# Kernel optimization log

Hardware: AMD Instinct MI355X
Metric: run time of the kernel (lower is better)

## Reference

```python
import jax, jax.numpy as jnp
import numpy as np

NEG_SLOPE = 0.2

def gatv2(x, edge_index, Wl, bl, Wr, br, att, bias):
    # PyG GATv2Conv (share_weights=False, add_self_loops=True, concat=True)
    N = x.shape[0]
    H, D = att.shape
    src0, dst0 = edge_index[0], edge_index[1]
    # remove_self_loops + add_self_loops semantics: mask existing self loops,
    # append one self loop per node (keeps static shapes under jit)
    loop = jnp.arange(N, dtype=src0.dtype)
    src = jnp.concatenate([src0, loop])
    dst = jnp.concatenate([dst0, loop])
    keep = jnp.concatenate([src0 != dst0, jnp.ones(N, dtype=bool)])  # drop original i->i edges
    xl = (x @ Wl + bl).reshape(N, H, D)  # source-side transform
    xr = (x @ Wr + br).reshape(N, H, D)  # target-side transform
    e = xl[src] + xr[dst]                                  # [E,H,D]
    logits = jnp.einsum('ehd,hd->eh', jax.nn.leaky_relu(e, NEG_SLOPE), att)
    logits = jnp.where(keep[:, None], logits, -jnp.inf)
    m = jax.ops.segment_max(logits, dst, num_segments=N)   # [N,H]
    ex = jnp.where(keep[:, None], jnp.exp(logits - m[dst]), 0.0)
    denom = jax.ops.segment_sum(ex, dst, num_segments=N)   # [N,H]
    alpha = ex / (denom[dst] + 1e-16)                      # [E,H]
    out = jax.ops.segment_sum(alpha[..., None] * xl[src], dst, num_segments=N)
    return out.reshape(N, H * D) + bias

def setup_inputs() -> dict:
    key = jax.random.key(0)
    ks = jax.random.split(key, 20)
    N, E, F, Hd = 50000, 400000, 5, 128
    s = 0.05
    inp = {
        'x': jax.random.normal(ks[0], (N, F), dtype=jnp.float32),
        'edge_index': jax.random.randint(ks[1], (2, E), 0, N, dtype=jnp.int64),
        # node_embed MLP
        'W1': jax.random.normal(ks[2], (F, Hd), dtype=jnp.float32) * s,
        'b1': jnp.zeros((Hd,), jnp.float32),
        'W2': jax.random.normal(ks[3], (Hd, Hd), dtype=jnp.float32) * s,
        'b2': jnp.zeros((Hd,), jnp.float32),
        # gnn1: GATv2Conv(128 -> 128, heads=4)
        'Wl1': jax.random.normal(ks[4], (Hd, 4 * Hd), dtype=jnp.float32) * s,
        'bl1': jnp.zeros((4 * Hd,), jnp.float32),
        'Wr1': jax.random.normal(ks[5], (Hd, 4 * Hd), dtype=jnp.float32) * s,
        'br1': jnp.zeros((4 * Hd,), jnp.float32),
        'att1': jax.random.normal(ks[6], (4, Hd), dtype=jnp.float32) * s,
        'bias1': jnp.zeros((4 * Hd,), jnp.float32),
        # gnn2: GATv2Conv(512 -> 128, heads=1)
        'Wl2': jax.random.normal(ks[7], (4 * Hd, Hd), dtype=jnp.float32) * s,
        'bl2': jnp.zeros((Hd,), jnp.float32),
        'Wr2': jax.random.normal(ks[8], (4 * Hd, Hd), dtype=jnp.float32) * s,
        'br2': jnp.zeros((Hd,), jnp.float32),
        'att2': jax.random.normal(ks[9], (1, Hd), dtype=jnp.float32) * s,
        'bias2': jnp.zeros((Hd,), jnp.float32),
    }
    return inp

def reference(x, edge_index, W1, b1, W2, b2, Wl1, bl1, Wr1, br1, att1, bias1,
              Wl2, bl2, Wr2, br2, att2, bias2):
    h = jax.nn.relu(x @ W1 + b1) @ W2 + b2                 # node_embed MLP
    h = jax.nn.relu(gatv2(h, edge_index, Wl1, bl1, Wr1, br1, att1, bias1))
    out = gatv2(h, edge_index, Wl2, bl2, Wr2, br2, att2, bias2)
    return out  # [N, 128]
```

## Files before the change

### kernel.cpp

```cpp
#include <hip/hip_runtime.h>
#include <math.h>

typedef __attribute__((ext_vector_type(8))) short bf16x8;
typedef __attribute__((ext_vector_type(4))) float f32x4;
typedef unsigned short ushort;
typedef unsigned int uint;

static __device__ __forceinline__ ushort f2bf(float f) {
    unsigned u = __float_as_uint(f);
    u = u + 0x7fff + ((u >> 16) & 1);
    return (ushort)(u >> 16);
}
static __device__ __forceinline__ float bf2f(ushort h) {
    return __uint_as_float(((unsigned)h) << 16);
}


__global__ void k_count(const int* __restrict__ src, const int* __restrict__ dst,
                        int E, int* __restrict__ counts) {
    int e = blockIdx.x * blockDim.x + threadIdx.x;
    if (e < E) {
        int s = src[e], d = dst[e];
        if (s != d) atomicAdd(&counts[d], 1);
    }
}

__global__ __launch_bounds__(256) void k_blocksum(const int* __restrict__ counts, int N,
                                                  int* __restrict__ bsum) {
    __shared__ int s[256];
    int t = threadIdx.x, i = blockIdx.x * 256 + t;
    s[t] = (i < N) ? counts[i] : 0;
    __syncthreads();
    for (int off = 128; off > 0; off >>= 1) {
        if (t < off) s[t] += s[t + off];
        __syncthreads();
    }
    if (t == 0) bsum[blockIdx.x] = s[0];
}

__global__ __launch_bounds__(256) void k_scanblocks(const int* __restrict__ bsum, int NB,
                                                    int* __restrict__ boff,
                                                    int* __restrict__ rowptr, int N) {
    __shared__ int s[256];
    int t = threadIdx.x;
    int v = (t < NB) ? bsum[t] : 0;
    s[t] = v;
    __syncthreads();
    for (int off = 1; off < 256; off <<= 1) {
        int u = (t >= off) ? s[t - off] : 0;
        __syncthreads();
        s[t] += u;
        __syncthreads();
    }
    if (t < NB) boff[t] = s[t] - v;
    if (t == NB - 1) rowptr[N] = s[t] + N;
}

__global__ __launch_bounds__(256) void k_scatter(const int* __restrict__ counts, int N,
                                                 const int* __restrict__ boff,
                                                 int* __restrict__ rowptr,
                                                 int* __restrict__ cursor) {
    __shared__ int s[256];
    int t = threadIdx.x, i = blockIdx.x * 256 + t;
    int c = (i < N) ? counts[i] : 0;
    s[t] = c;
    __syncthreads();
    for (int off = 1; off < 256; off <<= 1) {
        int u = (t >= off) ? s[t - off] : 0;
        __syncthreads();
        s[t] += u;
        __syncthreads();
    }
    if (i < N) {
        int excl = boff[blockIdx.x] + s[t] - c + i;
        rowptr[i] = excl;
        cursor[i] = excl;
    }
}

__global__ void k_fill(const int* __restrict__ src, const int* __restrict__ dst,
                       int E, int N, int* __restrict__ cursor, int* __restrict__ colA) {
    int i = blockIdx.x * blockDim.x + threadIdx.x;
    if (i < E) {
        int s = src[i], d = dst[i];
        if (s != d) { int p = atomicAdd(&cursor[d], 1); colA[p] = s; }
    } else if (i < E + N) {
        int n = i - E;
        int p = atomicAdd(&cursor[n], 1); colA[p] = n;
    }
}


__global__ __launch_bounds__(256) void k_repack(
    const float* __restrict__ W2, const float* __restrict__ Wl1,
    const float* __restrict__ Wr1, const float* __restrict__ Wl2,
    const float* __restrict__ Wr2,
    ushort* __restrict__ wfh, ushort* __restrict__ wfl)
{
    int job = blockIdx.y;
    int t = blockIdx.x * 256 + threadIdx.x;
    int ks = t >> 9, n = (t >> 6) & 7, l = t & 63;

    const float* W; int ldw, rowoff, col0;
    if (job == 0)      { W = W2;  ldw = 128; rowoff = 0;              col0 = 0; }
    else if (job < 5)  { W = Wl1; ldw = 512; rowoff = 0;              col0 = (job - 1) * 128; }
    else if (job < 9)  { W = Wr1; ldw = 512; rowoff = 0;              col0 = (job - 5) * 128; }
    else if (job < 13) { W = Wl2; ldw = 128; rowoff = (job - 9) * 128;  col0 = 0; }
    else               { W = Wr2; ldw = 128; rowoff = (job - 13) * 128; col0 = 0; }

    int krow = rowoff + ks * 32 + (l >> 4) * 8;
    int col = col0 + n * 16 + (l & 15);
    size_t dbase = (size_t)job * 16384 + (((size_t)(ks * 8 + n)) * 64 + l) * 8;
#pragma unroll
    for (int j = 0; j < 8; j++) {
        float v = W[(size_t)(krow + j) * ldw + col];
        ushort h = f2bf(v);
        ushort lo = f2bf(v - bf2f(h));
        wfh[dbase + j] = h;
        wfl[dbase + j] = lo;
    }
}


__global__ __launch_bounds__(256) void k_mlp1(
    const float* __restrict__ x, const float* __restrict__ W1, const float* __restrict__ b1,
    ushort* __restrict__ out, int N)
{
    int n = blockIdx.x * 2 + (threadIdx.x >> 7);
    int j = threadIdx.x & 127;
    if (n >= N) return;
    float s = b1[j];
#pragma unroll
    for (int k = 0; k < 5; k++) s = fmaf(x[(size_t)n * 5 + k], W1[k * 128 + j], s);
    s = fmaxf(s, 0.f);
    out[(size_t)n * 128 + j] = f2bf(s);
}


__global__ __launch_bounds__(256) void gemm_h0(
    const ushort* __restrict__ A,
    const ushort* __restrict__ wfh, const ushort* __restrict__ wfl,
    const float* __restrict__ bias,
    ushort* __restrict__ C, int M)
{
    int tid = threadIdx.x;
    int w = tid >> 6, l = tid & 63;
    int m0 = blockIdx.x * 128 + w * 32;
    int lr = l & 15, kg = l >> 4;

    f32x4 acc[2][8];
#pragma unroll
    for (int i = 0; i < 2; i++)
#pragma unroll
        for (int j = 0; j < 8; j++) acc[i][j] = (f32x4){0.f, 0.f, 0.f, 0.f};

    int row0 = m0 + lr, row1 = m0 + 16 + lr;
    bool ok0 = row0 < M, ok1 = row1 < M;
    const bf16x8 zz = {0, 0, 0, 0, 0, 0, 0, 0};

#pragma unroll
    for (int ks = 0; ks < 4; ks++) {
        int koff = ks * 32 + kg * 8;
        bf16x8 a0 = ok0 ? *(const bf16x8*)(A + (size_t)row0 * 128 + koff) : zz;
        bf16x8 a1 = ok1 ? *(const bf16x8*)(A + (size_t)row1 * 128 + koff) : zz;
#pragma unroll
        for (int n = 0; n < 8; n++) {
            size_t bo = (((size_t)(ks * 8 + n)) * 64 + l) * 8;
            bf16x8 bh = *(const bf16x8*)(wfh + bo);
            bf16x8 bl = *(const bf16x8*)(wfl + bo);
            acc[0][n] = __builtin_amdgcn_mfma_f32_16x16x32_bf16(a0, bh, acc[0][n], 0, 0, 0);
            acc[0][n] = __builtin_amdgcn_mfma_f32_16x16x32_bf16(a0, bl, acc[0][n], 0, 0, 0);
            acc[1][n] = __builtin_amdgcn_mfma_f32_16x16x32_bf16(a1, bh, acc[1][n], 0, 0, 0);
            acc[1][n] = __builtin_amdgcn_mfma_f32_16x16x32_bf16(a1, bl, acc[1][n], 0, 0, 0);
        }
    }

#pragma unroll
    for (int mf = 0; mf < 2; mf++) {
#pragma unroll
        for (int r = 0; r < 4; r++) {
            int row = m0 + mf * 16 + kg * 4 + r;
            if (row >= M) continue;
#pragma unroll
            for (int n = 0; n < 8; n++) {
                size_t idx = (size_t)row * 128 + n * 16 + lr;
                C[idx] = f2bf(acc[mf][n][r] + bias[n * 16 + lr]);
            }
        }
    }
}


__global__ __launch_bounds__(256) void gemm_xlr1(
    const ushort* __restrict__ A,
    const ushort* __restrict__ wh, const ushort* __restrict__ wl,
    const float* __restrict__ bl1, const float* __restrict__ br1,
    ushort* __restrict__ out, int M)
{
    int t = blockIdx.y;
    int tid = threadIdx.x;
    int w = tid >> 6, l = tid & 63;
    int m0 = blockIdx.x * 128 + w * 32;
    int lr = l & 15, kg = l >> 4;

    const ushort* bh_base = wh + (size_t)t * 16384;
    const ushort* bl_base = wl + (size_t)t * 16384;

    f32x4 acc[2][8];
#pragma unroll
    for (int i = 0; i < 2; i++)
#pragma unroll
        for (int j = 0; j < 8; j++) acc[i][j] = (f32x4){0.f, 0.f, 0.f, 0.f};

    int row0 = m0 + lr, row1 = m0 + 16 + lr;
    bool ok0 = row0 < M, ok1 = row1 < M;
    const bf16x8 zz = {0, 0, 0, 0, 0, 0, 0, 0};

#pragma unroll
    for (int ks = 0; ks < 4; ks++) {
        int koff = ks * 32 + kg * 8;
        bf16x8 a0 = ok0 ? *(const bf16x8*)(A + (size_t)row0 * 128 + koff) : zz;
        bf16x8 a1 = ok1 ? *(const bf16x8*)(A + (size_t)row1 * 128 + koff) : zz;
#pragma unroll
        for (int n = 0; n < 8; n++) {
            size_t bo = (((size_t)(ks * 8 + n)) * 64 + l) * 8;
            bf16x8 bh = *(const bf16x8*)(bh_base + bo);
            bf16x8 bl = *(const bf16x8*)(bl_base + bo);
            acc[0][n] = __builtin_amdgcn_mfma_f32_16x16x32_bf16(a0, bh, acc[0][n], 0, 0, 0);
            acc[0][n] = __builtin_amdgcn_mfma_f32_16x16x32_bf16(a0, bl, acc[0][n], 0, 0, 0);
            acc[1][n] = __builtin_amdgcn_mfma_f32_16x16x32_bf16(a1, bh, acc[1][n], 0, 0, 0);
            acc[1][n] = __builtin_amdgcn_mfma_f32_16x16x32_bf16(a1, bl, acc[1][n], 0, 0, 0);
        }
    }

    float bcol[8];
#pragma unroll
    for (int n = 0; n < 8; n++)
        bcol[n] = (t < 4) ? bl1[t * 128 + n * 16 + lr] : br1[(t - 4) * 128 + n * 16 + lr];

#pragma unroll
    for (int mf = 0; mf < 2; mf++) {
#pragma unroll
        for (int r = 0; r < 4; r++) {
            int row = m0 + mf * 16 + kg * 4 + r;
            if (row >= M) continue;
#pragma unroll
            for (int n = 0; n < 8; n++)
                out[(size_t)row * 1024 + t * 128 + n * 16 + lr] = f2bf(acc[mf][n][r] + bcol[n]);
        }
    }
}


__global__ __launch_bounds__(256) void gemm_xlr2(
    const ushort* __restrict__ A,
    const ushort* __restrict__ wfh, const ushort* __restrict__ wfl,
    const float* __restrict__ bl2, const float* __restrict__ br2,
    ushort* __restrict__ xl2, ushort* __restrict__ xr2, int M)
{
    int t = blockIdx.y;
    int tid = threadIdx.x;
    int w = tid >> 6, l = tid & 63;
    int m0 = blockIdx.x * 128 + w * 32;
    int lr = l & 15, kg = l >> 4;

    f32x4 acc[2][8];
#pragma unroll
    for (int i = 0; i < 2; i++)
#pragma unroll
        for (int j = 0; j < 8; j++) acc[i][j] = (f32x4){0.f, 0.f, 0.f, 0.f};

    int row0 = m0 + lr, row1 = m0 + 16 + lr;
    bool ok0 = row0 < M, ok1 = row1 < M;
    const bf16x8 zz = {0, 0, 0, 0, 0, 0, 0, 0};

    for (int kc = 0; kc < 4; kc++) {
        const ushort* bh_base = wfh + (size_t)(9 + t * 4 + kc) * 16384;
        const ushort* bl_base = wfl + (size_t)(9 + t * 4 + kc) * 16384;
        bf16x8 a0[4], a1[4];
#pragma unroll
        for (int ks = 0; ks < 4; ks++) {
            int koff = kc * 128 + ks * 32 + kg * 8;
            a0[ks] = ok0 ? *(const bf16x8*)(A + (size_t)row0 * 512 + koff) : zz;
            a1[ks] = ok1 ? *(const bf16x8*)(A + (size_t)row1 * 512 + koff) : zz;
        }
#pragma unroll
        for (int ks = 0; ks < 4; ks++) {
#pragma unroll
            for (int n = 0; n < 8; n++) {
                size_t bo = (((size_t)(ks * 8 + n)) * 64 + l) * 8;
                bf16x8 bh = *(const bf16x8*)(bh_base + bo);
                bf16x8 bl = *(const bf16x8*)(bl_base + bo);
                acc[0][n] = __builtin_amdgcn_mfma_f32_16x16x32_bf16(a0[ks], bh, acc[0][n], 0, 0, 0);
                acc[0][n] = __builtin_amdgcn_mfma_f32_16x16x32_bf16(a0[ks], bl, acc[0][n], 0, 0, 0);
                acc[1][n] = __builtin_amdgcn_mfma_f32_16x16x32_bf16(a1[ks], bh, acc[1][n], 0, 0, 0);
                acc[1][n] = __builtin_amdgcn_mfma_f32_16x16x32_bf16(a1[ks], bl, acc[1][n], 0, 0, 0);
            }
        }
    }

    const float* bias = (t == 0) ? bl2 : br2;
    ushort* outp = (t == 0) ? xl2 : xr2;

#pragma unroll
    for (int mf = 0; mf < 2; mf++) {
#pragma unroll
        for (int r = 0; r < 4; r++) {
            int row = m0 + mf * 16 + kg * 4 + r;
            if (row >= M) continue;
#pragma unroll
            for (int n = 0; n < 8; n++) {
                int col = n * 16 + lr;
                outp[(size_t)row * 128 + col] = f2bf(acc[mf][n][r] + bias[col]);
            }
        }
    }
}


__global__ __launch_bounds__(256) void gat_edge4(
    const ushort* __restrict__ xlr,
    const float* __restrict__ att,
    const float* __restrict__ bias,
    const int* __restrict__ rowptr, const int* __restrict__ colA,
    ushort* __restrict__ h1,
    int N)
{
    int n = blockIdx.x;
    int h = threadIdx.x >> 6, l = threadIdx.x & 63;
    int g = l >> 4, q = l & 15;

    const ushort* xlbase = xlr + h * 128 + q * 8;

    bf16x8 xrv = *(const bf16x8*)(xlr + (size_t)n * 1024 + (4 + h) * 128 + q * 8);
    float4 ata = *(const float4*)(att + h * 128 + q * 8);
    float4 atb = *(const float4*)(att + h * 128 + q * 8 + 4);
    float xr[8] , at[8] = {ata.x, ata.y, ata.z, ata.w, atb.x, atb.y, atb.z, atb.w};
#pragma unroll
    for (int j = 0; j < 8; j++) xr[j] = bf2f((ushort)xrv[j]);

    auto dotc = [&](bf16x8 v8, float* vv) -> float {
        float c = 0.f;
#pragma unroll
        for (int j = 0; j < 8; j++) {
            vv[j] = bf2f((ushort)v8[j]);
            float t = vv[j] + xr[j];
            t = (t > 0.f) ? t : 0.2f * t;
            c = fmaf(t, at[j], c);
        }
        c += __shfl_xor(c, 1);
        c += __shfl_xor(c, 2);
        c += __shfl_xor(c, 4);
        c += __shfl_xor(c, 8);
        return c;
    };

    float tmp[8];
    bf16x8 vself = *(const bf16x8*)(xlbase + (size_t)n * 1024);
    float cs = dotc(vself, tmp);

    int k0 = rowptr[n], k1 = rowptr[n + 1];
    float s = 0.f, o[8];
#pragma unroll
    for (int j = 0; j < 8; j++) o[j] = 0.f;

    auto edge = [&](bf16x8 v8) {
        float vv[8];
        float c = dotc(v8, vv);
        float p = __expf(fminf(c - cs, 80.f));
        s += p;
#pragma unroll
        for (int j = 0; j < 8; j++) o[j] = fmaf(p, vv[j], o[j]);
    };

    for (int base = k0 + g; base < k1; base += 16) {
        int x0 = colA[base];
        int x1 = (base + 4  < k1) ? colA[base + 4]  : -1;
        int x2 = (base + 8  < k1) ? colA[base + 8]  : -1;
        int x3 = (base + 12 < k1) ? colA[base + 12] : -1;
        int y1 = (x1 >= 0) ? x1 : n;
        int y2 = (x2 >= 0) ? x2 : n;
        int y3 = (x3 >= 0) ? x3 : n;
        bf16x8 v0 = *(const bf16x8*)(xlbase + (size_t)x0 * 1024);
        bf16x8 v1 = *(const bf16x8*)(xlbase + (size_t)y1 * 1024);
        bf16x8 v2 = *(const bf16x8*)(xlbase + (size_t)y2 * 1024);
        bf16x8 v3 = *(const bf16x8*)(xlbase + (size_t)y3 * 1024);
        edge(v0);
        if (x1 >= 0) edge(v1);
        if (x2 >= 0) edge(v2);
        if (x3 >= 0) edge(v3);
    }

#pragma unroll
    for (int off = 16; off <= 32; off <<= 1) {
        s += __shfl_xor(s, off);
#pragma unroll
        for (int j = 0; j < 8; j++) o[j] += __shfl_xor(o[j], off);
    }

    if (g == 0) {
        float inv = 1.f / (s + 1e-16f);
        float4 ba = *(const float4*)(bias + h * 128 + q * 8);
        float4 bb = *(const float4*)(bias + h * 128 + q * 8 + 4);
        float bs[8] = {ba.x, ba.y, ba.z, ba.w, bb.x, bb.y, bb.z, bb.w};
        bf16x8 pk;
#pragma unroll
        for (int j = 0; j < 8; j++)
            pk[j] = (short)f2bf(fmaxf(o[j] * inv + bs[j], 0.f));
        *(bf16x8*)(h1 + (size_t)n * 512 + h * 128 + q * 8) = pk;
    }
}


__global__ __launch_bounds__(256) void gat_edge1(
    const ushort* __restrict__ xl, const ushort* __restrict__ xr,
    const float* __restrict__ att, const float* __restrict__ bias,
    const int* __restrict__ rowptr, const int* __restrict__ colA,
    float* __restrict__ out, int N)
{
    int n = blockIdx.x * 4 + (threadIdx.x >> 6);
    if (n >= N) return;
    int l = threadIdx.x & 63;
    int g = l >> 4, q = l & 15;

    const ushort* xlbase = xl + q * 8;

    bf16x8 xrv = *(const bf16x8*)(xr + (size_t)n * 128 + q * 8);
    float4 ata = *(const float4*)(att + q * 8);
    float4 atb = *(const float4*)(att + q * 8 + 4);
    float xrr[8], at[8] = {ata.x, ata.y, ata.z, ata.w, atb.x, atb.y, atb.z, atb.w};
#pragma unroll
    for (int j = 0; j < 8; j++) xrr[j] = bf2f((ushort)xrv[j]);

    auto dotc = [&](bf16x8 v8, float* vv) -> float {
        float c = 0.f;
#pragma unroll
        for (int j = 0; j < 8; j++) {
            vv[j] = bf2f((ushort)v8[j]);
            float t = vv[j] + xrr[j];
            t = (t > 0.f) ? t : 0.2f * t;
            c = fmaf(t, at[j], c);
        }
        c += __shfl_xor(c, 1);
        c += __shfl_xor(c, 2);
        c += __shfl_xor(c, 4);
        c += __shfl_xor(c, 8);
        return c;
    };

    float tmp[8];
    bf16x8 vself = *(const bf16x8*)(xlbase + (size_t)n * 128);
    float cs = dotc(vself, tmp);

    int k0 = rowptr[n], k1 = rowptr[n + 1];
    float s = 0.f, o[8];
#pragma unroll
    for (int j = 0; j < 8; j++) o[j] = 0.f;

    auto edge = [&](bf16x8 v8) {
        float vv[8];
        float c = dotc(v8, vv);
        float p = __expf(fminf(c - cs, 80.f));
        s += p;
#pragma unroll
        for (int j = 0; j < 8; j++) o[j] = fmaf(p, vv[j], o[j]);
    };

    for (int base = k0 + g; base < k1; base += 16) {
        int x0 = colA[base];
        int x1 = (base + 4  < k1) ? colA[base + 4]  : -1;
        int x2 = (base + 8  < k1) ? colA[base + 8]  : -1;
        int x3 = (base + 12 < k1) ? colA[base + 12] : -1;
        int y1 = (x1 >= 0) ? x1 : n;
        int y2 = (x2 >= 0) ? x2 : n;
        int y3 = (x3 >= 0) ? x3 : n;
        bf16x8 v0 = *(const bf16x8*)(xlbase + (size_t)x0 * 128);
        bf16x8 v1 = *(const bf16x8*)(xlbase + (size_t)y1 * 128);
        bf16x8 v2 = *(const bf16x8*)(xlbase + (size_t)y2 * 128);
        bf16x8 v3 = *(const bf16x8*)(xlbase + (size_t)y3 * 128);
        edge(v0);
        if (x1 >= 0) edge(v1);
        if (x2 >= 0) edge(v2);
        if (x3 >= 0) edge(v3);
    }

#pragma unroll
    for (int off = 16; off <= 32; off <<= 1) {
        s += __shfl_xor(s, off);
#pragma unroll
        for (int j = 0; j < 8; j++) o[j] += __shfl_xor(o[j], off);
    }

    if (g == 0) {
        float inv = 1.f / (s + 1e-16f);
        float4 ba = *(const float4*)(bias + q * 8);
        float4 bb = *(const float4*)(bias + q * 8 + 4);
        float4 r0, r1;
        r0.x = o[0] * inv + ba.x;  r0.y = o[1] * inv + ba.y;
        r0.z = o[2] * inv + ba.z;  r0.w = o[3] * inv + ba.w;
        r1.x = o[4] * inv + bb.x;  r1.y = o[5] * inv + bb.y;
        r1.z = o[6] * inv + bb.z;  r1.w = o[7] * inv + bb.w;
        *(float4*)(out + (size_t)n * 128 + q * 8)     = r0;
        *(float4*)(out + (size_t)n * 128 + q * 8 + 4) = r1;
    }
}


extern "C" void kernel_launch(void* const* d_in, const int* in_sizes, int n_in,
                              void* d_out, int out_size, void* d_ws, size_t ws_size,
                              hipStream_t stream) {
    const float* x    = (const float*)d_in[0];
    const int* ei     = (const int*)d_in[1];
    const float* W1   = (const float*)d_in[2];
    const float* b1   = (const float*)d_in[3];
    const float* W2   = (const float*)d_in[4];
    const float* b2   = (const float*)d_in[5];
    const float* Wl1  = (const float*)d_in[6];
    const float* bl1  = (const float*)d_in[7];
    const float* Wr1  = (const float*)d_in[8];
    const float* br1  = (const float*)d_in[9];
    const float* att1 = (const float*)d_in[10];
    const float* bias1= (const float*)d_in[11];
    const float* Wl2  = (const float*)d_in[12];
    const float* bl2  = (const float*)d_in[13];
    const float* Wr2  = (const float*)d_in[14];
    const float* br2  = (const float*)d_in[15];
    const float* att2 = (const float*)d_in[16];
    const float* bias2= (const float*)d_in[17];

    int E = in_sizes[1] / 2;
    int N = in_sizes[0] / 5;
    const int* srcE = ei;
    const int* dstE = ei + E;

    float* dout = (float*)d_out;

    ushort* xlr1 = (ushort*)d_ws;
    ushort* h1   = xlr1 + (size_t)N * 1024;
    ushort* h0   = h1 + (size_t)N * 512;
    ushort* xr2  = h0 + (size_t)N * 128;
    ushort* wfh  = xr2 + (size_t)N * 128;
    ushort* wfl  = wfh + 17 * 16384;
    int* rowptr = (int*)(wfl + 17 * 16384);
    int* cursor = rowptr + (N + 1);
    int* counts = cursor + N;
    int* colA   = counts + N;
    int* bsum   = colA + (E + N);
    int* boff   = bsum + 256;

    ushort* cC  = h1;
    ushort* xl2 = h0;

    int NB = (N + 255) / 256;

    hipMemsetAsync(counts, 0, (size_t)N * sizeof(int), stream);
    k_count<<<(E + 255) / 256, 256, 0, stream>>>(srcE, dstE, E, counts);
    k_blocksum <<<NB, 256, 0, stream>>>(counts, N, bsum);
    k_scanblocks<<<1, 256, 0, stream>>>(bsum, NB, boff, rowptr, N);
    k_scatter  <<<NB, 256, 0, stream>>>(counts, N, boff, rowptr, cursor);
    k_fill <<<(E + N + 255) / 256, 256, 0, stream>>>(srcE, dstE, E, N, cursor, colA);

    {
        dim3 g(8, 17);
        k_repack<<<g, 256, 0, stream>>>(W2, Wl1, Wr1, Wl2, Wr2, wfh, wfl);
    }

    int mb128 = (N + 127) / 128;

    k_mlp1<<<(N + 1) / 2, 256, 0, stream>>>(x, W1, b1, cC, N);
    gemm_h0<<<mb128, 256, 0, stream>>>(cC, wfh, wfl, b2, h0, N);

    {
        dim3 g(mb128, 8);
        gemm_xlr1<<<g, 256, 0, stream>>>(h0, wfh + 16384, wfl + 16384, bl1, br1, xlr1, N);
    }
    gat_edge4<<<N, 256, 0, stream>>>(xlr1, att1, bias1, rowptr, colA, h1, N);

    {
        dim3 g(mb128, 2);
        gemm_xlr2<<<g, 256, 0, stream>>>(h1, wfh, wfl, bl2, br2, xl2, xr2, N);
    }
    gat_edge1<<<(N + 3) / 4, 256, 0, stream>>>(xl2, xr2, att2, bias2, rowptr, colA, dout, N);
}
```

Baseline: 406.1 us.

## Fuse MLP first layer into h0 GEMM and restructure xlr GEMM grids

```diff
diff --git a/kernel.cpp b/kernel.cpp
--- a/kernel.cpp
+++ b/kernel.cpp
@@ -122,25 +122,10 @@
 }
 
 
-__global__ __launch_bounds__(256) void k_mlp1(
+__global__ __launch_bounds__(256) void k_mlp_h0(
     const float* __restrict__ x, const float* __restrict__ W1, const float* __restrict__ b1,
-    ushort* __restrict__ out, int N)
-{
-    int n = blockIdx.x * 2 + (threadIdx.x >> 7);
-    int j = threadIdx.x & 127;
-    if (n >= N) return;
-    float s = b1[j];
-#pragma unroll
-    for (int k = 0; k < 5; k++) s = fmaf(x[(size_t)n * 5 + k], W1[k * 128 + j], s);
-    s = fmaxf(s, 0.f);
-    out[(size_t)n * 128 + j] = f2bf(s);
-}
-
-
-__global__ __launch_bounds__(256) void gemm_h0(
-    const ushort* __restrict__ A,
     const ushort* __restrict__ wfh, const ushort* __restrict__ wfl,
-    const float* __restrict__ bias,
+    const float* __restrict__ b2,
     ushort* __restrict__ C, int M)
 {
     int tid = threadIdx.x;
@@ -148,30 +133,54 @@
     int m0 = blockIdx.x * 128 + w * 32;
     int lr = l & 15, kg = l >> 4;
 
+    int row0 = m0 + lr, row1 = row0 + 16;
+    bool ok0 = row0 < M, ok1 = row1 < M;
+
+    float x0[5], x1[5];
+#pragma unroll
+    for (int k = 0; k < 5; k++) {
+        x0[k] = ok0 ? x[(size_t)row0 * 5 + k] : 0.f;
+        x1[k] = ok1 ? x[(size_t)row1 * 5 + k] : 0.f;
+    }
+
+    bf16x8 a0[4], a1[4];
+#pragma unroll
+    for (int ks = 0; ks < 4; ks++) {
+#pragma unroll
+        for (int j = 0; j < 8; j++) {
+            int col = ks * 32 + kg * 8 + j;
+            float wc[5];
+#pragma unroll
+            for (int k = 0; k < 5; k++) wc[k] = W1[k * 128 + col];
+            float bb = b1[col];
+            float h0v = bb, h1v = bb;
+#pragma unroll
+            for (int k = 0; k < 5; k++) {
+                h0v = fmaf(x0[k], wc[k], h0v);
+                h1v = fmaf(x1[k], wc[k], h1v);
+            }
+            a0[ks][j] = (short)f2bf(fmaxf(h0v, 0.f));
+            a1[ks][j] = (short)f2bf(fmaxf(h1v, 0.f));
+        }
+    }
+
     f32x4 acc[2][8];
 #pragma unroll
     for (int i = 0; i < 2; i++)
 #pragma unroll
         for (int j = 0; j < 8; j++) acc[i][j] = (f32x4){0.f, 0.f, 0.f, 0.f};
 
-    int row0 = m0 + lr, row1 = m0 + 16 + lr;
-    bool ok0 = row0 < M, ok1 = row1 < M;
-    const bf16x8 zz = {0, 0, 0, 0, 0, 0, 0, 0};
-
 #pragma unroll
     for (int ks = 0; ks < 4; ks++) {
-        int koff = ks * 32 + kg * 8;
-        bf16x8 a0 = ok0 ? *(const bf16x8*)(A + (size_t)row0 * 128 + koff) : zz;
-        bf16x8 a1 = ok1 ? *(const bf16x8*)(A + (size_t)row1 * 128 + koff) : zz;
 #pragma unroll
         for (int n = 0; n < 8; n++) {
             size_t bo = (((size_t)(ks * 8 + n)) * 64 + l) * 8;
             bf16x8 bh = *(const bf16x8*)(wfh + bo);
             bf16x8 bl = *(const bf16x8*)(wfl + bo);
-            acc[0][n] = __builtin_amdgcn_mfma_f32_16x16x32_bf16(a0, bh, acc[0][n], 0, 0, 0);
-            acc[0][n] = __builtin_amdgcn_mfma_f32_16x16x32_bf16(a0, bl, acc[0][n], 0, 0, 0);
-            acc[1][n] = __builtin_amdgcn_mfma_f32_16x16x32_bf16(a1, bh, acc[1][n], 0, 0, 0);
-            acc[1][n] = __builtin_amdgcn_mfma_f32_16x16x32_bf16(a1, bl, acc[1][n], 0, 0, 0);
+            acc[0][n] = __builtin_amdgcn_mfma_f32_16x16x32_bf16(a0[ks], bh, acc[0][n], 0, 0, 0);
+            acc[0][n] = __builtin_amdgcn_mfma_f32_16x16x32_bf16(a0[ks], bl, acc[0][n], 0, 0, 0);
+            acc[1][n] = __builtin_amdgcn_mfma_f32_16x16x32_bf16(a1[ks], bh, acc[1][n], 0, 0, 0);
+            acc[1][n] = __builtin_amdgcn_mfma_f32_16x16x32_bf16(a1[ks], bl, acc[1][n], 0, 0, 0);
         }
     }
 
@@ -184,7 +193,7 @@
 #pragma unroll
             for (int n = 0; n < 8; n++) {
                 size_t idx = (size_t)row * 128 + n * 16 + lr;
-                C[idx] = f2bf(acc[mf][n][r] + bias[n * 16 + lr]);
+                C[idx] = f2bf(acc[mf][n][r] + b2[n * 16 + lr]);
             }
         }
     }
@@ -197,93 +206,33 @@
     const float* __restrict__ bl1, const float* __restrict__ br1,
     ushort* __restrict__ out, int M)
 {
-    int t = blockIdx.y;
     int tid = threadIdx.x;
     int w = tid >> 6, l = tid & 63;
     int m0 = blockIdx.x * 128 + w * 32;
     int lr = l & 15, kg = l >> 4;
 
-    const ushort* bh_base = wh + (size_t)t * 16384;
-    const ushort* bl_base = wl + (size_t)t * 16384;
-
-    f32x4 acc[2][8];
-#pragma unroll
-    for (int i = 0; i < 2; i++)
-#pragma unroll
-        for (int j = 0; j < 8; j++) acc[i][j] = (f32x4){0.f, 0.f, 0.f, 0.f};
-
-    int row0 = m0 + lr, row1 = m0 + 16 + lr;
+    int row0 = m0 + lr, row1 = row0 + 16;
     bool ok0 = row0 < M, ok1 = row1 < M;
     const bf16x8 zz = {0, 0, 0, 0, 0, 0, 0, 0};
 
+    bf16x8 a0[4], a1[4];
 #pragma unroll
     for (int ks = 0; ks < 4; ks++) {
         int koff = ks * 32 + kg * 8;
-        bf16x8 a0 = ok0 ? *(const bf16x8*)(A + (size_t)row0 * 128 + koff) : zz;
-        bf16x8 a1 = ok1 ? *(const bf16x8*)(A + (size_t)row1 * 128 + koff) : zz;
-#pragma unroll
-        for (int n = 0; n < 8; n++) {
-            size_t bo = (((size_t)(ks * 8 + n)) * 64 + l) * 8;
-            bf16x8 bh = *(const bf16x8*)(bh_base + bo);
-            bf16x8 bl = *(const bf16x8*)(bl_base + bo);
-            acc[0][n] = __builtin_amdgcn_mfma_f32_16x16x32_bf16(a0, bh, acc[0][n], 0, 0, 0);
-            acc[0][n] = __builtin_amdgcn_mfma_f32_16x16x32_bf16(a0, bl, acc[0][n], 0, 0, 0);
-            acc[1][n] = __builtin_amdgcn_mfma_f32_16x16x32_bf16(a1, bh, acc[1][n], 0, 0, 0);
-            acc[1][n] = __builtin_amdgcn_mfma_f32_16x16x32_bf16(a1, bl, acc[1][n], 0, 0, 0);
-        }
-    }
-
-    float bcol[8];
-#pragma unroll
-    for (int n = 0; n < 8; n++)
-        bcol[n] = (t < 4) ? bl1[t * 128 + n * 16 + lr] : br1[(t - 4) * 128 + n * 16 + lr];
-
-#pragma unroll
-    for (int mf = 0; mf < 2; mf++) {
-#pragma unroll
-        for (int r = 0; r < 4; r++) {
-            int row = m0 + mf * 16 + kg * 4 + r;
-            if (row >= M) continue;
-#pragma unroll
-            for (int n = 0; n < 8; n++)
-                out[(size_t)row * 1024 + t * 128 + n * 16 + lr] = f2bf(acc[mf][n][r] + bcol[n]);
-        }
-    }
-}
-
-
-__global__ __launch_bounds__(256) void gemm_xlr2(
-    const ushort* __restrict__ A,
-    const ushort* __restrict__ wfh, const ushort* __restrict__ wfl,
-    const float* __restrict__ bl2, const float* __restrict__ br2,
-    ushort* __restrict__ xl2, ushort* __restrict__ xr2, int M)
-{
-    int t = blockIdx.y;
-    int tid = threadIdx.x;
-    int w = tid >> 6, l = tid & 63;
-    int m0 = blockIdx.x * 128 + w * 32;
-    int lr = l & 15, kg = l >> 4;
-
-    f32x4 acc[2][8];
-#pragma unroll
-    for (int i = 0; i < 2; i++)
-#pragma unroll
-        for (int j = 0; j < 8; j++) acc[i][j] = (f32x4){0.f, 0.f, 0.f, 0.f};
-
-    int row0 = m0 + lr, row1 = m0 + 16 + lr;
-    bool ok0 = row0 < M, ok1 = row1 < M;
-    const bf16x8 zz = {0, 0, 0, 0, 0, 0, 0, 0};
-
-    for (int kc = 0; kc < 4; kc++) {
-        const ushort* bh_base = wfh + (size_t)(9 + t * 4 + kc) * 16384;
-        const ushort* bl_base = wfl + (size_t)(9 + t * 4 + kc) * 16384;
-        bf16x8 a0[4], a1[4];
-#pragma unroll
-        for (int ks = 0; ks < 4; ks++) {
-            int koff = kc * 128 + ks * 32 + kg * 8;
-            a0[ks] = ok0 ? *(const bf16x8*)(A + (size_t)row0 * 512 + koff) : zz;
-            a1[ks] = ok1 ? *(const bf16x8*)(A + (size_t)row1 * 512 + koff) : zz;
-        }
+        a0[ks] = ok0 ? *(const bf16x8*)(A + (size_t)row0 * 128 + koff) : zz;
+        a1[ks] = ok1 ? *(const bf16x8*)(A + (size_t)row1 * 128 + koff) : zz;
+    }
+
+    for (int t = 0; t < 8; t++) {
+        const ushort* bh_base = wh + (size_t)t * 16384;
+        const ushort* bl_base = wl + (size_t)t * 16384;
+
+        f32x4 acc[2][8];
+#pragma unroll
+        for (int i = 0; i < 2; i++)
+#pragma unroll
+            for (int j = 0; j < 8; j++) acc[i][j] = (f32x4){0.f, 0.f, 0.f, 0.f};
+
 #pragma unroll
         for (int ks = 0; ks < 4; ks++) {
 #pragma unroll
@@ -297,22 +246,81 @@
                 acc[1][n] = __builtin_amdgcn_mfma_f32_16x16x32_bf16(a1[ks], bl, acc[1][n], 0, 0, 0);
             }
         }
-    }
-
-    const float* bias = (t == 0) ? bl2 : br2;
-    ushort* outp = (t == 0) ? xl2 : xr2;
-
-#pragma unroll
-    for (int mf = 0; mf < 2; mf++) {
-#pragma unroll
-        for (int r = 0; r < 4; r++) {
-            int row = m0 + mf * 16 + kg * 4 + r;
-            if (row >= M) continue;
-#pragma unroll
-            for (int n = 0; n < 8; n++) {
-                int col = n * 16 + lr;
-                outp[(size_t)row * 128 + col] = f2bf(acc[mf][n][r] + bias[col]);
+
+        float bcol[8];
+#pragma unroll
+        for (int n = 0; n < 8; n++)
+            bcol[n] = (t < 4) ? bl1[t * 128 + n * 16 + lr] : br1[(t - 4) * 128 + n * 16 + lr];
+
+#pragma unroll
+        for (int mf = 0; mf < 2; mf++) {
+#pragma unroll
+            for (int r = 0; r < 4; r++) {
+                int row = m0 + mf * 16 + kg * 4 + r;
+                if (row >= M) continue;
+#pragma unroll
+                for (int n = 0; n < 8; n++)
+                    out[(size_t)row * 1024 + t * 128 + n * 16 + lr] = f2bf(acc[mf][n][r] + bcol[n]);
             }
+        }
+    }
+}
+
+
+__global__ __launch_bounds__(256) void gemm_xlr2(
+    const ushort* __restrict__ A,
+    const ushort* __restrict__ wfh, const ushort* __restrict__ wfl,
+    const float* __restrict__ bl2, const float* __restrict__ br2,
+    ushort* __restrict__ xl2, ushort* __restrict__ xr2, int M)
+{
+    int tid = threadIdx.x;
+    int w = tid >> 6, l = tid & 63;
+    int m0 = blockIdx.x * 64 + w * 16;
+    int lr = l & 15, kg = l >> 4;
+
+    int row0 = m0 + lr;
+    bool ok0 = row0 < M;
+    const bf16x8 zz = {0, 0, 0, 0, 0, 0, 0, 0};
+
+    f32x4 acc[2][8];
+#pragma unroll
+    for (int i = 0; i < 2; i++)
+#pragma unroll
+        for (int j = 0; j < 8; j++) acc[i][j] = (f32x4){0.f, 0.f, 0.f, 0.f};
+
+    for (int kc = 0; kc < 4; kc++) {
+        bf16x8 ah[4];
+#pragma unroll
+        for (int ks = 0; ks < 4; ks++)
+            ah[ks] = ok0 ? *(const bf16x8*)(A + (size_t)row0 * 512 + kc * 128 + ks * 32 + kg * 8) : zz;
+
+#pragma unroll
+        for (int t = 0; t < 2; t++) {
+            const ushort* bh_base = wfh + (size_t)(9 + t * 4 + kc) * 16384;
+            const ushort* bl_base = wfl + (size_t)(9 + t * 4 + kc) * 16384;
+#pragma unroll
+            for (int ks = 0; ks < 4; ks++) {
+#pragma unroll
+                for (int n = 0; n < 8; n++) {
+                    size_t bo = (((size_t)(ks * 8 + n)) * 64 + l) * 8;
+                    bf16x8 bh = *(const bf16x8*)(bh_base + bo);
+                    bf16x8 bl = *(const bf16x8*)(bl_base + bo);
+                    acc[t][n] = __builtin_amdgcn_mfma_f32_16x16x32_bf16(ah[ks], bh, acc[t][n], 0, 0, 0);
+                    acc[t][n] = __builtin_amdgcn_mfma_f32_16x16x32_bf16(ah[ks], bl, acc[t][n], 0, 0, 0);
+                }
+            }
+        }
+    }
+
+#pragma unroll
+    for (int r = 0; r < 4; r++) {
+        int row = m0 + kg * 4 + r;
+        if (row >= M) continue;
+#pragma unroll
+        for (int n = 0; n < 8; n++) {
+            int col = n * 16 + lr;
+            xl2[(size_t)row * 128 + col] = f2bf(acc[0][n][r] + bl2[col]);
+            xr2[(size_t)row * 128 + col] = f2bf(acc[1][n][r] + br2[col]);
         }
     }
 }
@@ -548,7 +556,6 @@
     int* bsum   = colA + (E + N);
     int* boff   = bsum + 256;
 
-    ushort* cC  = h1;
     ushort* xl2 = h0;
 
     int NB = (N + 255) / 256;
@@ -566,19 +573,13 @@
     }
 
     int mb128 = (N + 127) / 128;
-
-    k_mlp1<<<(N + 1) / 2, 256, 0, stream>>>(x, W1, b1, cC, N);
-    gemm_h0<<<mb128, 256, 0, stream>>>(cC, wfh, wfl, b2, h0, N);
-
-    {
-        dim3 g(mb128, 8);
-        gemm_xlr1<<<g, 256, 0, stream>>>(h0, wfh + 16384, wfl + 16384, bl1, br1, xlr1, N);
-    }
+    int mb64  = (N + 63) / 64;
+
+    k_mlp_h0<<<mb128, 256, 0, stream>>>(x, W1, b1, wfh, wfl, b2, h0, N);
+
+    gemm_xlr1<<<mb128, 256, 0, stream>>>(h0, wfh + 16384, wfl + 16384, bl1, br1, xlr1, N);
     gat_edge4<<<N, 256, 0, stream>>>(xlr1, att1, bias1, rowptr, colA, h1, N);
 
-    {
-        dim3 g(mb128, 2);
-        gemm_xlr2<<<g, 256, 0, stream>>>(h1, wfh, wfl, bl2, br2, xl2, xr2, N);
-    }
+    gemm_xlr2<<<mb64, 256, 0, stream>>>(h1, wfh, wfl, bl2, br2, xl2, xr2, N);
     gat_edge1<<<(N + 3) / 4, 256, 0, stream>>>(xl2, xr2, att2, bias2, rowptr, colA, dout, N);
 }
```

Measured after the change: 389.1 us. 1.04x faster.
